# Kernel tuning notes

Measured on AMD Instinct MI355X. Metric: run time of the kernel, lower is better.

The kernel has to match this reference:

```python
import jax, jax.numpy as jnp
import numpy as np

D_MODEL = 512
N_QUBITS = 10
N_LAYERS = 2
N_TOKENS = 16384
DIM = 2 ** N_QUBITS


def _rx(t):
    c = jnp.cos(t / 2) + 0j
    s = -1j * jnp.sin(t / 2)
    return jnp.stack([jnp.stack([c, s]), jnp.stack([s, c])]).astype(jnp.complex64)


def _ry(t):
    c = jnp.cos(t / 2) + 0j
    s = jnp.sin(t / 2) + 0j
    return jnp.stack([jnp.stack([c, -s]), jnp.stack([s, c])]).astype(jnp.complex64)


def _rz(t):
    z = jnp.zeros((), jnp.complex64)
    return jnp.stack([jnp.stack([jnp.exp(-1j * t / 2), z]),
                      jnp.stack([z, jnp.exp(1j * t / 2)])]).astype(jnp.complex64)


def _apply_1q(state, q, U, n):
    # state: [B, 2^n]; qubit 0 is the most significant bit
    B = state.shape[0]
    s = state.reshape(B, 2 ** q, 2, 2 ** (n - q - 1))
    s = jnp.einsum('ij,bajk->baik', U, s)
    return s.reshape(B, 2 ** n)


def _simulate(psi, rot, ent, n):
    # psi: [B, 2^n] complex64. rot: [L, n, 3]. ent: [L, n-1].
    L = rot.shape[0]
    idx = jnp.arange(2 ** n)
    for l in range(L):
        for q in range(n):
            psi = _apply_1q(psi, q, _rx(rot[l, q, 0]), n)
            psi = _apply_1q(psi, q, _ry(rot[l, q, 1]), n)
            psi = _apply_1q(psi, q, _rz(rot[l, q, 2]), n)
        for i in range(n - 1):  # nearest-neighbor parameterized CZ (controlled-phase)
            q1, q2 = i, i + 1
            both = (((idx >> (n - 1 - q1)) & 1) & ((idx >> (n - 1 - q2)) & 1)) == 1
            phase = jnp.where(both, jnp.exp(1j * ent[l, i].astype(jnp.complex64)),
                              jnp.ones((), jnp.complex64))
            psi = psi * phase
    return psi


def setup_inputs() -> dict:
    key = jax.random.key(0)
    ks = jax.random.split(key, 6)
    return {
        'x': jax.random.normal(ks[0], (N_TOKENS, D_MODEL), jnp.float32),
        'W_in': jax.random.normal(ks[1], (DIM, D_MODEL), jnp.float32) / np.sqrt(D_MODEL),
        'b_in': jnp.zeros((DIM,), jnp.float32),
        'W_out': jax.random.normal(ks[2], (D_MODEL, DIM), jnp.float32) / np.sqrt(DIM),
        'b_out': jnp.zeros((D_MODEL,), jnp.float32),
        'rot': jax.random.normal(ks[3], (N_LAYERS, N_QUBITS, 3), jnp.float32),
        'ent': jax.random.normal(ks[4], (N_LAYERS, N_QUBITS - 1), jnp.float32),
        'ln_w': jnp.ones((D_MODEL,), jnp.float32),
        'ln_b': jnp.zeros((D_MODEL,), jnp.float32),
    }


def reference(x, W_in, b_in, W_out, b_out, rot, ent, ln_w, ln_b):
    n = rot.shape[1]
    # input projection to 2^n amplitudes, then L2-normalize (F.normalize, eps=1e-12)
    xq = x @ W_in.T + b_in
    norm = jnp.maximum(jnp.linalg.norm(xq, axis=-1, keepdims=True), 1e-12)
    psi = (xq / norm).astype(jnp.complex64)
    psi = _simulate(psi, rot, ent, n)
    probs = (psi.real ** 2 + psi.imag ** 2).astype(x.dtype)  # |amp|^2
    out = probs @ W_out.T + b_out
    # LayerNorm(d_model), eps=1e-5
    mu = jnp.mean(out, axis=-1, keepdims=True)
    var = jnp.mean((out - mu) ** 2, axis=-1, keepdims=True)
    return (out - mu) / jnp.sqrt(var + 1e-5) * ln_w + ln_b
```

## Files before the change

### kernel.cpp

```cpp
#include <hip/hip_runtime.h>
#include <cstdint>

#define TOKENS 16384
#define DMODEL 512
#define DIM    1024
#define NQ     10
#define NL     2
#define BM     128
#define BN     128
#define BK     32

typedef __bf16 bf16x8 __attribute__((ext_vector_type(8)));
typedef float  f32x4  __attribute__((ext_vector_type(4)));
typedef unsigned short u16x8 __attribute__((ext_vector_type(8)));

__device__ __forceinline__ float b2f(unsigned short h) {
    union { unsigned u; float f; } v; v.u = ((unsigned)h) << 16; return v.f;
}
__device__ __forceinline__ unsigned short f2b(float f) {
    unsigned u = __builtin_bit_cast(unsigned, f);
    return (unsigned short)((u + 0x7FFFu + ((u >> 16) & 1u)) >> 16);
}
__device__ __forceinline__ float2 cmul(float2 a, float2 b) {
    return make_float2(a.x * b.x - a.y * b.y, a.x * b.y + a.y * b.x);
}
__device__ __forceinline__ float2 cadd(float2 a, float2 b) {
    return make_float2(a.x + b.x, a.y + b.y);
}
__device__ __forceinline__ void async_copy16(const void* g, void* l) {
    __builtin_amdgcn_global_load_lds((const __attribute__((address_space(1))) void*)g,
                                     (__attribute__((address_space(3))) void*)l, 16, 0, 0);
}

__global__ __launch_bounds__(256)
void prep_all_kernel(const float* __restrict__ x,  unsigned short* __restrict__ xb,
                     const float* __restrict__ w2, unsigned short* __restrict__ w2b,
                     const float* __restrict__ W_in, unsigned short* __restrict__ wtT,
                     const float* __restrict__ rot, const float* __restrict__ ent,
                     const float* __restrict__ bin,
                     unsigned short* __restrict__ U, float* __restrict__ b2) {
    const int bid = blockIdx.x;
    const int t = threadIdx.x;

    if (bid < 256) {
        __shared__ float2 Gs[NL * NQ * 4];
        const int lane = t & 63;
        const int c = bid * 4 + (t >> 6);

        if (t < NL * NQ) {
            float tx = rot[t * 3 + 0] * 0.5f;
            float ty = rot[t * 3 + 1] * 0.5f;
            float tz = rot[t * 3 + 2] * 0.5f;
            float cx = cosf(tx), sx = sinf(tx);
            float cy = cosf(ty), sy = sinf(ty);
            float cz = cosf(tz), sz = sinf(tz);
            float2 rx00 = make_float2(cx, 0.f),  rx01 = make_float2(0.f, -sx);
            float2 rx10 = make_float2(0.f, -sx), rx11 = make_float2(cx, 0.f);
            float2 ry00 = make_float2(cy, 0.f),  ry01 = make_float2(-sy, 0.f);
            float2 ry10 = make_float2(sy, 0.f),  ry11 = make_float2(cy, 0.f);
            float2 m00 = cadd(cmul(ry00, rx00), cmul(ry01, rx10));
            float2 m01 = cadd(cmul(ry00, rx01), cmul(ry01, rx11));
            float2 m10 = cadd(cmul(ry10, rx00), cmul(ry11, rx10));
            float2 m11 = cadd(cmul(ry10, rx01), cmul(ry11, rx11));
            float2 e0 = make_float2(cz, -sz), e1 = make_float2(cz, sz);
            Gs[t * 4 + 0] = cmul(e0, m00);
            Gs[t * 4 + 1] = cmul(e0, m01);
            Gs[t * 4 + 2] = cmul(e1, m10);
            Gs[t * 4 + 3] = cmul(e1, m11);
        }
        float ef[NL * (NQ - 1)];
        #pragma unroll
        for (int i = 0; i < NL * (NQ - 1); i++) ef[i] = ent[i];
        __syncthreads();

        float2 amp[16];
        #pragma unroll
        for (int r = 0; r < 16; r++)
            amp[r] = make_float2((lane * 16 + r == c) ? 1.f : 0.f, 0.f);

        #pragma unroll 1
        for (int li = 0; li < NL; li++) {
            const int l = NL - 1 - li;
            #pragma unroll
            for (int r = 0; r < 16; r++) {
                int idx = lane * 16 + r;
                float ang = 0.f;
                #pragma unroll
                for (int q = 0; q < NQ - 1; q++) {
                    int both = ((idx >> (9 - q)) & 1) & ((idx >> (8 - q)) & 1);
                    if (both) ang += ef[l * (NQ - 1) + q];
                }
                amp[r] = cmul(amp[r], make_float2(cosf(ang), sinf(ang)));
            }
            const float2* Gl = Gs + l * NQ * 4;
            #pragma unroll
            for (int qq = 0; qq < NQ; qq++) {
                const int q = 9 - qq;
                float2 u00 = Gl[q * 4 + 0], u10 = Gl[q * 4 + 1];
                float2 u01 = Gl[q * 4 + 2], u11 = Gl[q * 4 + 3];
                if (q >= 6) {
                    const int S = 1 << (9 - q);
                    #pragma unroll
                    for (int r = 0; r < 16; r++) {
                        if (r & S) continue;
                        float2 a = amp[r], b = amp[r + S];
                        float2 n0, n1;
                        n0.x = u00.x * a.x - u00.y * a.y + u01.x * b.x - u01.y * b.y;
                        n0.y = u00.x * a.y + u00.y * a.x + u01.x * b.y + u01.y * b.x;
                        n1.x = u10.x * a.x - u10.y * a.y + u11.x * b.x - u11.y * b.y;
                        n1.y = u10.x * a.y + u10.y * a.x + u11.x * b.y + u11.y * b.x;
                        amp[r] = n0; amp[r + S] = n1;
                    }
                } else {
                    const int mask = 32 >> q;
                    int bit = (lane >> (5 - q)) & 1;
                    float2 ua = bit ? u11 : u00;
                    float2 ub = bit ? u10 : u01;
                    #pragma unroll
                    for (int r = 0; r < 16; r++) {
                        float px = __shfl_xor(amp[r].x, mask, 64);
                        float py = __shfl_xor(amp[r].y, mask, 64);
                        float nx = ua.x * amp[r].x - ua.y * amp[r].y + ub.x * px - ub.y * py;
                        float ny = ua.x * amp[r].y + ua.y * amp[r].x + ub.x * py + ub.y * px;
                        amp[r] = make_float2(nx, ny);
                    }
                }
            }
        }

        float accRe = 0.f, accIm = 0.f;
        #pragma unroll
        for (int i = 0; i < 4; i++) {
            float4 bv = *(const float4*)&bin[lane * 16 + i * 4];
            accRe += amp[i * 4 + 0].x * bv.x + amp[i * 4 + 1].x * bv.y
                   + amp[i * 4 + 2].x * bv.z + amp[i * 4 + 3].x * bv.w;
            accIm += amp[i * 4 + 0].y * bv.x + amp[i * 4 + 1].y * bv.y
                   + amp[i * 4 + 2].y * bv.z + amp[i * 4 + 3].y * bv.w;
        }
        #pragma unroll
        for (int m = 1; m < 64; m <<= 1) {
            accRe += __shfl_xor(accRe, m, 64);
            accIm += __shfl_xor(accIm, m, 64);
        }
        const int nR = ((c >> 4) << 5) + (c & 15);
        if (lane == 0) { b2[nR] = accRe; b2[nR + 16] = accIm; }

        u16x8 o0, o1, p0, p1;
        #pragma unroll
        for (int r = 0; r < 8; r++) {
            o0[r] = f2b(amp[r].x);     o1[r] = f2b(amp[r + 8].x);
            p0[r] = f2b(amp[r].y);     p1[r] = f2b(amp[r + 8].y);
        }
        unsigned short* rowRe = U + (size_t)nR * DIM + lane * 16;
        unsigned short* rowIm = U + (size_t)(nR + 16) * DIM + lane * 16;
        *(u16x8*)rowRe = o0; *(u16x8*)(rowRe + 8) = o1;
        *(u16x8*)rowIm = p0; *(u16x8*)(rowIm + 8) = p1;
        return;
    }

    if (bid < 768) {
        __shared__ float tile[32][33];
        const int b2i = bid - 256;
        const int tx = t & 31, ty = t >> 5;
        const int d0 = (b2i & 15) * 32, j0 = (b2i >> 4) * 32;
        #pragma unroll
        for (int i = 0; i < 32; i += 8)
            tile[ty + i][tx] = W_in[(size_t)(j0 + ty + i) * DMODEL + d0 + tx];
        __syncthreads();
        #pragma unroll
        for (int i = 0; i < 32; i += 8)
            wtT[(size_t)(d0 + ty + i) * DIM + j0 + tx] = f2b(tile[tx][ty + i]);
        return;
    }

    const int NX4 = TOKENS * DMODEL / 4;
    const int NW4 = DMODEL * DIM / 4;
    const int total = NX4 + NW4;
    const int stride = 2048 * 256;
    for (int i = (bid - 768) * 256 + t; i < total; i += stride) {
        const float* s; unsigned short* d; int j;
        if (i < NX4) { s = x;  d = xb;  j = i; }
        else         { s = w2; d = w2b; j = i - NX4; }
        float4 v = *(const float4*)&s[(size_t)j * 4];
        ushort4 o;
        o.x = f2b(v.x); o.y = f2b(v.y); o.z = f2b(v.z); o.w = f2b(v.w);
        *(ushort4*)&d[(size_t)j * 4] = o;
    }
}

__global__ __launch_bounds__(256)
void fold_kernel(const unsigned short* __restrict__ A, const unsigned short* __restrict__ B,
                 unsigned short* __restrict__ C) {
    __shared__ unsigned short lds_a[BM * BK];
    __shared__ unsigned short lds_b[BN * BK];
    const int t = threadIdx.x;
    const int wave = t >> 6, lane = t & 63;
    const int wm = wave >> 1, wn = wave & 1;
    const int bm0 = blockIdx.y * BM;
    const int bn0 = blockIdx.x * BN;
    const int K = DIM, N = DMODEL;

    f32x4 acc[4][4] = {};
    const int c0 = t, c1 = t + 256;
    const int r0 = c0 >> 2, g0 = (c0 & 3) ^ ((r0 >> 1) & 3);
    const int r1 = c1 >> 2, g1 = (c1 & 3) ^ ((r1 >> 1) & 3);

    for (int k0 = 0; k0 < K; k0 += BK) {
        async_copy16(A + (size_t)(bm0 + r0) * K + k0 + g0 * 8, (char*)lds_a + wave * 1024);
        async_copy16(A + (size_t)(bm0 + r1) * K + k0 + g1 * 8, (char*)lds_a + wave * 1024 + 4096);
        async_copy16(B + (size_t)(bn0 + r0) * K + k0 + g0 * 8, (char*)lds_b + wave * 1024);
        async_copy16(B + (size_t)(bn0 + r1) * K + k0 + g1 * 8, (char*)lds_b + wave * 1024 + 4096);
        __syncthreads();

        bf16x8 af[4], bfr[4];
        #pragma unroll
        for (int i = 0; i < 4; i++) {
            int row = wm * 64 + i * 16 + (lane & 15);
            int slot = (lane >> 4) ^ ((row >> 1) & 3);
            af[i] = *(const bf16x8*)&lds_a[row * BK + slot * 8];
            int nrow = wn * 64 + i * 16 + (lane & 15);
            int nslot = (lane >> 4) ^ ((nrow >> 1) & 3);
            bfr[i] = *(const bf16x8*)&lds_b[nrow * BK + nslot * 8];
        }
        #pragma unroll
        for (int i = 0; i < 4; i++)
            #pragma unroll
            for (int j = 0; j < 4; j++)
                acc[i][j] = __builtin_amdgcn_mfma_f32_16x16x32_bf16(af[i], bfr[j], acc[i][j], 0, 0, 0);
        __syncthreads();
    }

    #pragma unroll
    for (int i = 0; i < 4; i++)
        #pragma unroll
        for (int j = 0; j < 4; j++) {
            int col = bn0 + wn * 64 + j * 16 + (lane & 15);
            #pragma unroll
            for (int r = 0; r < 4; r++) {
                int row = bm0 + wm * 64 + i * 16 + (lane >> 4) * 4 + r;
                C[(size_t)row * N + col] = f2b(acc[i][j][r]);
            }
        }
}

__global__ __launch_bounds__(512, 2)
void gemm1_kernel(const unsigned short* __restrict__ A, const unsigned short* __restrict__ B,
                  const float* __restrict__ bias, unsigned short* __restrict__ P) {
    const int K = DMODEL;
    __shared__ unsigned short sm[2 * 32768];
    const int t = threadIdx.x;
    const int wave = t >> 6, lane = t & 63;
    const int wm = wave >> 2, wn = wave & 3;
    const int laneR = lane & 15;

    const int bid = blockIdx.x;
    const int swz = (bid & 7) * 64 + (bid >> 3);
    const int bm0 = (swz >> 3) * 256;
    const int bn0 = (swz & 7) * 256;

    const int csrc = (t & 3) ^ ((t >> 3) & 3);
    const int rowg = t >> 2;
    const unsigned aOff0 = (unsigned)(bm0 + rowg) * DMODEL + csrc * 8;
    const unsigned aOff1 = (unsigned)(bm0 + 128 + rowg) * DMODEL + csrc * 8;
    const unsigned bOff0 = (unsigned)(bn0 + rowg) * DMODEL + csrc * 8;
    const unsigned bOff1 = (unsigned)(bn0 + 128 + rowg) * DMODEL + csrc * 8;

    const int slotc = (((lane >> 4) ^ ((lane >> 1) & 3)) & 3) * 8;

    f32x4 acc[8][4] = {};

    #define G1_STAGE(nbuf, kk, kb)                                                 \
    {                                                                              \
        unsigned short* d0 = sm + (nbuf) * 32768 + (kk) * 8192 + wave * 512;       \
        async_copy16(A + aOff0 + (kb) + (kk) * 32, d0);                            \
        async_copy16(A + aOff1 + (kb) + (kk) * 32, d0 + 4096);                     \
        async_copy16(B + bOff0 + (kb) + (kk) * 32, d0 + 16384);                    \
        async_copy16(B + bOff1 + (kb) + (kk) * 32, d0 + 20480);                    \
    }

    #define G1_COMPUTE(cbuf, kk)                                                   \
    {                                                                              \
        const unsigned short* la = sm + (cbuf) * 32768 + (kk) * 8192;              \
        const unsigned short* lb = la + 16384;                                     \
        bf16x8 af[8], bfr[4];                                                      \
        _Pragma("unroll")                                                          \
        for (int i = 0; i < 8; i++)                                                \
            af[i] = *(const bf16x8*)&la[(wm * 128 + i * 16 + laneR) * 32 + slotc]; \
        _Pragma("unroll")                                                          \
        for (int j = 0; j < 4; j++)                                                \
            bfr[j] = *(const bf16x8*)&lb[(wn * 64 + j * 16 + laneR) * 32 + slotc]; \
        __builtin_amdgcn_s_setprio(1);                                             \
        _Pragma("unroll")                                                          \
        for (int i = 0; i < 8; i++)                                                \
            _Pragma("unroll")                                                      \
            for (int j = 0; j < 4; j++)                                            \
                acc[i][j] = __builtin_amdgcn_mfma_f32_16x16x32_bf16(af[i], bfr[j], acc[i][j], 0, 0, 0); \
        __builtin_amdgcn_s_setprio(0);                                             \
    }

    G1_STAGE(0, 0, 0);
    G1_STAGE(0, 1, 0);
    asm volatile("s_waitcnt vmcnt(4)" ::: "memory");
    asm volatile("s_barrier" ::: "memory");

    const int NT = K / 64;
    #pragma unroll
    for (int kt = 0; kt < 7; kt++) {
        const int cur = kt & 1, nxt = cur ^ 1;
        const unsigned kb = (unsigned)(kt + 1) * 64;
        G1_STAGE(nxt, 0, kb);
        G1_COMPUTE(cur, 0);
        asm volatile("s_waitcnt vmcnt(4)" ::: "memory");
        asm volatile("s_barrier" ::: "memory");
        G1_STAGE(nxt, 1, kb);
        G1_COMPUTE(cur, 1);
        asm volatile("s_waitcnt vmcnt(4)" ::: "memory");
        asm volatile("s_barrier" ::: "memory");
    }
    G1_COMPUTE(1, 0);
    asm volatile("s_waitcnt vmcnt(0)" ::: "memory");
    asm volatile("s_barrier" ::: "memory");
    G1_COMPUTE(1, 1);
    (void)NT;

    #undef G1_STAGE
    #undef G1_COMPUTE

    #pragma unroll
    for (int i = 0; i < 8; i++) {
        #pragma unroll
        for (int jp = 0; jp < 2; jp++) {
            int colRe = bn0 + wn * 64 + jp * 32 + laneR;
            float bRe = bias[colRe];
            float bIm = bias[colRe + 16];
            int pc = (bn0 >> 1) + wn * 32 + jp * 16 + laneR;
            #pragma unroll
            for (int r = 0; r < 4; r++) {
                int row = bm0 + wm * 128 + i * 16 + (lane >> 4) * 4 + r;
                float vr = acc[i][2 * jp][r] + bRe;
                float vi = acc[i][2 * jp + 1][r] + bIm;
                P[(size_t)row * DIM + pc] = f2b(vr * vr + vi * vi);
            }
        }
    }
}

__global__ __launch_bounds__(512)
void gemm2_ln_kernel(const unsigned short* __restrict__ A,
                     const unsigned short* __restrict__ B,
                     const float* __restrict__ bias,
                     const float* __restrict__ lw, const float* __restrict__ lb,
                     float* __restrict__ out) {
    __shared__ unsigned short sm[2 * 36864];
    __shared__ float redS[4][64], redQ[4][64];
    __shared__ float muS[64], rsS[64], n2s[64];
    const int t = threadIdx.x, wave = t >> 6, lane = t & 63;
    const int wm = wave >> 2, wn = wave & 3;
    const int laneR = lane & 15;
    const int bm0 = blockIdx.x * 64;

    const int csrc = (t & 3) ^ ((t >> 3) & 3);
    const int akk  = t >> 8, arow = (t >> 2) & 63;
    const unsigned aSrc = (unsigned)(bm0 + arow) * DIM + akk * 32 + csrc * 8;
    const int brow = t >> 2;
    const int slotc = (((lane >> 4) ^ ((lane >> 1) & 3)) & 3) * 8;

    f32x4 acc[2][8] = {};
    f32x4 accN[2] = {};
    bf16x8 ones;
    #pragma unroll
    for (int r = 0; r < 8; r++) ones[r] = (__bf16)1.0f;

    #define G2_STAGE_A(nbuf, kb) {                                          \
        async_copy16(A + aSrc + (kb), sm + (nbuf) * 36864 + t * 8);         \
    }
    #define G2_STAGE_B(nbuf, kk, kb) {                                      \
        unsigned short* d = sm + (nbuf) * 36864 + 4096 + (kk) * 16384 + t * 8; \
        const unsigned short* s0 = B + (size_t)brow * DIM + (kb) + (kk) * 32 + csrc * 8; \
        async_copy16(s0,                 d);                                 \
        async_copy16(s0 + 128 * DIM,     d + 4096);                         \
        async_copy16(s0 + 256 * DIM,     d + 8192);                         \
        async_copy16(s0 + 384 * DIM,     d + 12288);                        \
    }
    #define G2_COMPUTE(cbuf, kk) {                                          \
        const unsigned short* la  = sm + (cbuf) * 36864 + (kk) * 2048;      \
        const unsigned short* lbp = sm + (cbuf) * 36864 + 4096 + (kk) * 16384; \
        bf16x8 af[2], bfr[8];                                               \
        _Pragma("unroll")                                                   \
        for (int i = 0; i < 2; i++)                                         \
            af[i] = *(const bf16x8*)&la[(wm * 32 + i * 16 + laneR) * 32 + slotc]; \
        _Pragma("unroll")                                                   \
        for (int j = 0; j < 8; j++)                                         \
            bfr[j] = *(const bf16x8*)&lbp[(wn * 128 + j * 16 + laneR) * 32 + slotc]; \
        __builtin_amdgcn_s_setprio(1);                                      \
        _Pragma("unroll")                                                   \
        for (int i = 0; i < 2; i++)                                         \
            _Pragma("unroll")                                               \
            for (int j = 0; j < 8; j++)                                     \
                acc[i][j] = __builtin_amdgcn_mfma_f32_16x16x32_bf16(af[i], bfr[j], acc[i][j], 0, 0, 0); \
        if (wn == 0) {                                                      \
            _Pragma("unroll")                                               \
            for (int i = 0; i < 2; i++)                                     \
                accN[i] = __builtin_amdgcn_mfma_f32_16x16x32_bf16(af[i], ones, accN[i], 0, 0, 0); \
        }                                                                   \
        __builtin_amdgcn_s_setprio(0);                                      \
    }

    G2_STAGE_A(0, 0); G2_STAGE_B(0, 0, 0); G2_STAGE_B(0, 1, 0);
    asm volatile("s_waitcnt vmcnt(4)" ::: "memory");
    asm volatile("s_barrier" ::: "memory");

    #pragma unroll
    for (int n = 0; n < 15; n++) {
        const int cb = n & 1, nb = cb ^ 1;
        const unsigned kb = (unsigned)(n + 1) * 64;
        G2_STAGE_A(nb, kb); G2_STAGE_B(nb, 0, kb);
        G2_COMPUTE(cb, 0);
        asm volatile("s_waitcnt vmcnt(5)" ::: "memory");
        asm volatile("s_barrier" ::: "memory");
        G2_STAGE_B(nb, 1, kb);
        G2_COMPUTE(cb, 1);
        asm volatile("s_waitcnt vmcnt(4)" ::: "memory");
        asm volatile("s_barrier" ::: "memory");
    }
    G2_COMPUTE(1, 0);
    asm volatile("s_waitcnt vmcnt(0)" ::: "memory");
    asm volatile("s_barrier" ::: "memory");
    G2_COMPUTE(1, 1);

    #undef G2_STAGE_A
    #undef G2_STAGE_B
    #undef G2_COMPUTE

    if (wn == 0 && laneR == 0) {
        #pragma unroll
        for (int i = 0; i < 2; i++)
            #pragma unroll
            for (int r = 0; r < 4; r++)
                n2s[wm * 32 + i * 16 + (lane >> 4) * 4 + r] = accN[i][r];
    }
    __syncthreads();

    float bvj[8];
    #pragma unroll
    for (int j = 0; j < 8; j++) bvj[j] = bias[wn * 128 + j * 16 + laneR];

    #pragma unroll
    for (int i = 0; i < 2; i++)
        #pragma unroll
        for (int r = 0; r < 4; r++) {
            int rl = wm * 32 + i * 16 + (lane >> 4) * 4 + r;
            float nn = 1.0f / fmaxf(n2s[rl], 1e-24f);
            float s = 0.f, q = 0.f;
            #pragma unroll
            for (int j = 0; j < 8; j++) {
                float val = acc[i][j][r] * nn + bvj[j];
                acc[i][j][r] = val;
                s += val; q += val * val;
            }
            s += __shfl_xor(s, 1, 64); q += __shfl_xor(q, 1, 64);
            s += __shfl_xor(s, 2, 64); q += __shfl_xor(q, 2, 64);
            s += __shfl_xor(s, 4, 64); q += __shfl_xor(q, 4, 64);
            s += __shfl_xor(s, 8, 64); q += __shfl_xor(q, 8, 64);
            if (laneR == 0) { redS[wn][rl] = s; redQ[wn][rl] = q; }
        }
    __syncthreads();
    if (t < 64) {
        float s = redS[0][t] + redS[1][t] + redS[2][t] + redS[3][t];
        float q = redQ[0][t] + redQ[1][t] + redQ[2][t] + redQ[3][t];
        float mu = s * (1.0f / DMODEL);
        float var = q * (1.0f / DMODEL) - mu * mu;
        muS[t] = mu;
        rsS[t] = rsqrtf(var + 1e-5f);
    }
    __syncthreads();
    #pragma unroll
    for (int i = 0; i < 2; i++)
        #pragma unroll
        for (int j = 0; j < 8; j++) {
            int col = wn * 128 + j * 16 + laneR;
            float w = lw[col], bb = lb[col];
            #pragma unroll
            for (int r = 0; r < 4; r++) {
                int rl = wm * 32 + i * 16 + (lane >> 4) * 4 + r;
                out[(size_t)(bm0 + rl) * DMODEL + col] =
                    (acc[i][j][r] - muS[rl]) * rsS[rl] * w + bb;
            }
        }
}

extern "C" void kernel_launch(void* const* d_in, const int* in_sizes, int n_in,
                              void* d_out, int out_size, void* d_ws, size_t ws_size,
                              hipStream_t stream) {
    (void)in_sizes; (void)n_in; (void)out_size; (void)ws_size;
    const float* x     = (const float*)d_in[0];
    const float* W_in  = (const float*)d_in[1];
    const float* b_in  = (const float*)d_in[2];
    const float* W_out = (const float*)d_in[3];
    const float* b_out = (const float*)d_in[4];
    const float* rot   = (const float*)d_in[5];
    const float* ent   = (const float*)d_in[6];
    const float* ln_w  = (const float*)d_in[7];
    const float* ln_b  = (const float*)d_in[8];
    float* out = (float*)d_out;

    char* ws = (char*)d_ws;
    unsigned short* p    = (unsigned short*)ws;
    unsigned short* x_bf = (unsigned short*)(ws + 33554432ull);
    unsigned short* wtT  = (unsigned short*)(ws + 50331648ull);
    unsigned short* w2b  = (unsigned short*)(ws + 51380224ull);
    unsigned short* Ucat = (unsigned short*)(ws + 52428800ull);
    unsigned short* W1c  = (unsigned short*)(ws + 56623104ull);
    float*          b2   = (float*)(ws + 58720256ull);

    prep_all_kernel<<<2816, 256, 0, stream>>>(x, x_bf, W_out, w2b, W_in, wtT,
                                              rot, ent, b_in, Ucat, b2);
    fold_kernel<<<dim3(DMODEL / BN, 2 * DIM / BM), 256, 0, stream>>>(Ucat, wtT, W1c);
    gemm1_kernel<<<512, 512, 0, stream>>>(x_bf, W1c, b2, p);
    gemm2_ln_kernel<<<TOKENS / 64, 512, 0, stream>>>(
        p, w2b, b_out, ln_w, ln_b, out);
}
```

Before: 202.5 us.

## Retile fold GEMM to 64x64 blocks with double-buffered BK=64 pipeline

The fold kernel (Ucat × W_in, a 2048x512x1024 GEMM) now uses 64x64 output tiles instead of 128x128, which raises the block count from 64 to 256 so more CUs are busy. It also double-buffers a BK=64 LDS stage with an XOR swizzle, so the next tile's async copies overlap the current tile's MFMAs. The cost is less data reuse per block and more global traffic, but this kernel is small compared with the main GEMMs, so the gain is limited to the fold stage.

```diff
diff --git a/kernel.cpp b/kernel.cpp
--- a/kernel.cpp
+++ b/kernel.cpp
@@ -191,54 +191,73 @@
 __global__ __launch_bounds__(256)
 void fold_kernel(const unsigned short* __restrict__ A, const unsigned short* __restrict__ B,
                  unsigned short* __restrict__ C) {
-    __shared__ unsigned short lds_a[BM * BK];
-    __shared__ unsigned short lds_b[BN * BK];
+    __shared__ unsigned short sm[2 * 8192];
     const int t = threadIdx.x;
     const int wave = t >> 6, lane = t & 63;
     const int wm = wave >> 1, wn = wave & 1;
-    const int bm0 = blockIdx.y * BM;
-    const int bn0 = blockIdx.x * BN;
-    const int K = DIM, N = DMODEL;
-
-    f32x4 acc[4][4] = {};
-    const int c0 = t, c1 = t + 256;
-    const int r0 = c0 >> 2, g0 = (c0 & 3) ^ ((r0 >> 1) & 3);
-    const int r1 = c1 >> 2, g1 = (c1 & 3) ^ ((r1 >> 1) & 3);
-
-    for (int k0 = 0; k0 < K; k0 += BK) {
-        async_copy16(A + (size_t)(bm0 + r0) * K + k0 + g0 * 8, (char*)lds_a + wave * 1024);
-        async_copy16(A + (size_t)(bm0 + r1) * K + k0 + g1 * 8, (char*)lds_a + wave * 1024 + 4096);
-        async_copy16(B + (size_t)(bn0 + r0) * K + k0 + g0 * 8, (char*)lds_b + wave * 1024);
-        async_copy16(B + (size_t)(bn0 + r1) * K + k0 + g1 * 8, (char*)lds_b + wave * 1024 + 4096);
+    const int laneR = lane & 15;
+    const int bm0 = blockIdx.y * 64;
+    const int bn0 = blockIdx.x * 64;
+
+    const int csrc = (t & 7) ^ ((t >> 3) & 7);
+    const int rowg = t >> 3;
+    const unsigned aOff0 = (unsigned)(bm0 + rowg) * DIM + csrc * 8;
+    const unsigned aOff1 = (unsigned)(bm0 + 32 + rowg) * DIM + csrc * 8;
+    const unsigned bOff0 = (unsigned)(bn0 + rowg) * DIM + csrc * 8;
+    const unsigned bOff1 = (unsigned)(bn0 + 32 + rowg) * DIM + csrc * 8;
+
+    f32x4 acc[2][2] = {};
+
+    #define F_STAGE(nbuf, kt) {                                            \
+        unsigned short* d = sm + (nbuf) * 8192 + t * 8;                    \
+        async_copy16(A + aOff0 + (kt) * 64, d);                            \
+        async_copy16(A + aOff1 + (kt) * 64, d + 2048);                     \
+        async_copy16(B + bOff0 + (kt) * 64, d + 4096);                     \
+        async_copy16(B + bOff1 + (kt) * 64, d + 6144);                     \
+    }
+
+    F_STAGE(0, 0);
+    asm volatile("s_waitcnt vmcnt(0)" ::: "memory");
+    __syncthreads();
+
+    #pragma unroll
+    for (int kt = 0; kt < 16; kt++) {
+        const int cur = kt & 1;
+        if (kt < 15) F_STAGE(cur ^ 1, kt + 1);
+        const unsigned short* la = sm + cur * 8192;
+        const unsigned short* lb = la + 4096;
+        #pragma unroll
+        for (int kk = 0; kk < 2; kk++) {
+            bf16x8 af[2], bfr[2];
+            #pragma unroll
+            for (int i = 0; i < 2; i++) {
+                int row = wm * 32 + i * 16 + laneR;
+                int slot = ((lane >> 4) + kk * 4) ^ (row & 7);
+                af[i] = *(const bf16x8*)&la[row * 64 + slot * 8];
+                int nrow = wn * 32 + i * 16 + laneR;
+                int nslot = ((lane >> 4) + kk * 4) ^ (nrow & 7);
+                bfr[i] = *(const bf16x8*)&lb[nrow * 64 + nslot * 8];
+            }
+            #pragma unroll
+            for (int i = 0; i < 2; i++)
+                #pragma unroll
+                for (int j = 0; j < 2; j++)
+                    acc[i][j] = __builtin_amdgcn_mfma_f32_16x16x32_bf16(af[i], bfr[j], acc[i][j], 0, 0, 0);
+        }
+        asm volatile("s_waitcnt vmcnt(0)" ::: "memory");
         __syncthreads();
-
-        bf16x8 af[4], bfr[4];
-        #pragma unroll
-        for (int i = 0; i < 4; i++) {
-            int row = wm * 64 + i * 16 + (lane & 15);
-            int slot = (lane >> 4) ^ ((row >> 1) & 3);
-            af[i] = *(const bf16x8*)&lds_a[row * BK + slot * 8];
-            int nrow = wn * 64 + i * 16 + (lane & 15);
-            int nslot = (lane >> 4) ^ ((nrow >> 1) & 3);
-            bfr[i] = *(const bf16x8*)&lds_b[nrow * BK + nslot * 8];
-        }
-        #pragma unroll
-        for (int i = 0; i < 4; i++)
-            #pragma unroll
-            for (int j = 0; j < 4; j++)
-                acc[i][j] = __builtin_amdgcn_mfma_f32_16x16x32_bf16(af[i], bfr[j], acc[i][j], 0, 0, 0);
-        __syncthreads();
-    }
-
-    #pragma unroll
-    for (int i = 0; i < 4; i++)
-        #pragma unroll
-        for (int j = 0; j < 4; j++) {
-            int col = bn0 + wn * 64 + j * 16 + (lane & 15);
+    }
+    #undef F_STAGE
+
+    #pragma unroll
+    for (int i = 0; i < 2; i++)
+        #pragma unroll
+        for (int j = 0; j < 2; j++) {
+            int col = bn0 + wn * 32 + j * 16 + laneR;
             #pragma unroll
             for (int r = 0; r < 4; r++) {
-                int row = bm0 + wm * 64 + i * 16 + (lane >> 4) * 4 + r;
-                C[(size_t)row * N + col] = f2b(acc[i][j][r]);
+                int row = bm0 + wm * 32 + i * 16 + (lane >> 4) * 4 + r;
+                C[(size_t)row * DMODEL + col] = f2b(acc[i][j][r]);
             }
         }
 }
@@ -303,7 +322,6 @@
     asm volatile("s_waitcnt vmcnt(4)" ::: "memory");
     asm volatile("s_barrier" ::: "memory");
 
-    const int NT = K / 64;
     #pragma unroll
     for (int kt = 0; kt < 7; kt++) {
         const int cur = kt & 1, nxt = cur ^ 1;
@@ -321,7 +339,6 @@
     asm volatile("s_waitcnt vmcnt(0)" ::: "memory");
     asm volatile("s_barrier" ::: "memory");
     G1_COMPUTE(1, 1);
-    (void)NT;
 
     #undef G1_STAGE
     #undef G1_COMPUTE
@@ -515,7 +532,7 @@
 
     prep_all_kernel<<<2816, 256, 0, stream>>>(x, x_bf, W_out, w2b, W_in, wtT,
                                               rot, ent, b_in, Ucat, b2);
-    fold_kernel<<<dim3(DMODEL / BN, 2 * DIM / BM), 256, 0, stream>>>(Ucat, wtT, W1c);
+    fold_kernel<<<dim3(DMODEL / 64, 2 * DIM / 64), 256, 0, stream>>>(Ucat, wtT, W1c);
     gemm1_kernel<<<512, 512, 0, stream>>>(x_bf, W1c, b2, p);
     gemm2_ln_kernel<<<TOKENS / 64, 512, 0, stream>>>(
         p, w2b, b_out, ln_w, ln_b, out);
```

Result: faster. 195.9 us (-3.3%).
